# Kernel optimization log

Hardware: AMD Instinct MI355X
Metric: run time of the kernel (lower is better)

Reference implementation:

```python
import jax, jax.numpy as jnp
import numpy as np

B, S, H, NH, HD = 2, 2048, 4096, 32, 128
THETA = 10000.0


def rotate_half(x):
    x1, x2 = jnp.split(x, 2, axis=-1)
    return jnp.concatenate((-x2, x1), axis=-1)


def setup_inputs() -> dict:
    key = jax.random.key(0)
    ks = jax.random.split(key, 6)
    hidden_states = jax.random.normal(ks[0], (B, S, H), dtype=jnp.float32)
    # additive causal mask, [1,1,S,S]
    causal = jnp.triu(jnp.full((S, S), -1e9, dtype=jnp.float32), k=1)
    attention_mask = causal[None, None, :, :]
    scale = 0.02
    Wq = jax.random.normal(ks[1], (H, H), dtype=jnp.float32) * scale
    Wk = jax.random.normal(ks[2], (H, H), dtype=jnp.float32) * scale
    Wv = jax.random.normal(ks[3], (H, H), dtype=jnp.float32) * scale
    Wo = jax.random.normal(ks[4], (H, H), dtype=jnp.float32) * scale
    return {"hidden_states": hidden_states, "attention_mask": attention_mask,
            "Wq": Wq, "Wk": Wk, "Wv": Wv, "Wo": Wo}


def _rope_tables(seq_len, dtype):
    inv_freq = 1.0 / (THETA ** (jnp.arange(0, HD, 2, dtype=jnp.float32) / HD))
    t = jnp.arange(seq_len, dtype=jnp.float32)
    freqs = jnp.einsum('i,j->ij', t, inv_freq)          # [S, HD/2]
    emb = jnp.concatenate((freqs, freqs), axis=-1)       # [S, HD]
    return jnp.cos(emb).astype(dtype), jnp.sin(emb).astype(dtype)


def reference(hidden_states, attention_mask, Wq, Wk, Wv, Wo):
    b, s, _ = hidden_states.shape
    # nn.Linear: y = x @ W.T
    q = jnp.einsum('bsh,oh->bso', hidden_states, Wq).reshape(b, s, NH, HD).transpose(0, 2, 1, 3)
    k = jnp.einsum('bsh,oh->bso', hidden_states, Wk).reshape(b, s, NH, HD).transpose(0, 2, 1, 3)
    v = jnp.einsum('bsh,oh->bso', hidden_states, Wv).reshape(b, s, NH, HD).transpose(0, 2, 1, 3)
    cos, sin = _rope_tables(s, q.dtype)                  # [S, HD] broadcast over b,h
    q = q * cos + rotate_half(q) * sin
    k = k * cos + rotate_half(k) * sin
    scores = jnp.einsum('bhqd,bhkd->bhqk', q, k) / jnp.sqrt(jnp.asarray(HD, q.dtype))
    scores = scores + attention_mask
    attn = jax.nn.softmax(scores.astype(jnp.float32), axis=-1).astype(q.dtype)
    out = jnp.einsum('bhqk,bhkd->bhqd', attn, v)
    out = out.transpose(0, 2, 1, 3).reshape(b, s, H)
    return jnp.einsum('bsh,oh->bso', out, Wo)
```

## Files before the change

kernel.cpp:

```cpp
#include <hip/hip_runtime.h>
#include <stdint.h>

typedef __attribute__((ext_vector_type(4))) float f32x4;
typedef __attribute__((ext_vector_type(8))) short bf16x8;
typedef __attribute__((ext_vector_type(4))) unsigned int u32x4;

__device__ __forceinline__ short f2bf(float x) {
  unsigned int u = __builtin_bit_cast(unsigned int, x);
  unsigned int r = (u + 0x7fffu + ((u >> 16) & 1u)) >> 16;
  return (short)r;
}
__device__ __forceinline__ float bf2f(short s) {
  unsigned int u = ((unsigned int)(unsigned short)s) << 16;
  return __builtin_bit_cast(float, u);
}
__device__ __forceinline__ unsigned pkbf(float lo, float hi) {
  unsigned r;
  asm("v_cvt_pk_bf16_f32 %0, %1, %2" : "=v"(r) : "v"(lo), "v"(hi));
  return r;
}

__device__ __forceinline__ void gload_lds16(const void* g, void* l) {
  __builtin_amdgcn_global_load_lds(
      (const __attribute__((address_space(1))) void*)g,
      (__attribute__((address_space(3))) void*)l, 16, 0, 0);
}

__global__ __launch_bounds__(256) void cvt4(const float* __restrict__ a,
                                            const float* __restrict__ b,
                                            const float* __restrict__ c,
                                            const float* __restrict__ d,
                                            short* __restrict__ oa,
                                            short* __restrict__ ob,
                                            short* __restrict__ oc,
                                            short* __restrict__ od, int n) {
  const float* in = (blockIdx.y == 0) ? a : (blockIdx.y == 1) ? b : (blockIdx.y == 2) ? c : d;
  short* out = (blockIdx.y == 0) ? oa : (blockIdx.y == 1) ? ob : (blockIdx.y == 2) ? oc : od;
  int idx = blockIdx.x * blockDim.x + threadIdx.x;
  int stride = gridDim.x * blockDim.x;
  for (int i = idx * 4; i < n; i += stride * 4) {
    float4 v = *(const float4*)(in + i);
    short4 o;
    o.x = f2bf(v.x); o.y = f2bf(v.y); o.z = f2bf(v.z); o.w = f2bf(v.w);
    *(short4*)(out + i) = o;
  }
}

__global__ __launch_bounds__(256) void cvt_bf16(const float* __restrict__ in,
                                                short* __restrict__ out, int n) {
  int idx = blockIdx.x * blockDim.x + threadIdx.x;
  int stride = gridDim.x * blockDim.x;
  for (int i = idx * 4; i < n; i += stride * 4) {
    float4 v = *(const float4*)(in + i);
    short4 o;
    o.x = f2bf(v.x); o.y = f2bf(v.y); o.z = f2bf(v.z); o.w = f2bf(v.w);
    *(short4*)(out + i) = o;
  }
}

__global__ __launch_bounds__(256) void rope_table_k(float2* __restrict__ tab) {
  int idx = blockIdx.x * 256 + threadIdx.x;
  int s = idx >> 6, j = idx & 63;
  float invf = powf(10000.0f, -((float)j) / 64.0f);
  float a = (float)s * invf;
  tab[idx] = make_float2(cosf(a), sinf(a));
}

__global__ __launch_bounds__(256) void rope_apply_k(short* __restrict__ Qb,
                                                    short* __restrict__ Kb,
                                                    const float2* __restrict__ tab) {
  bool isK = (blockIdx.y != 0);
  short* base = isK ? Kb : Qb;
  float post = isK ? 1.0f : (0.08838834764831845f * 1.4426950408889634f);
  int token = blockIdx.x;
  int s = token & 2047;
  short* rowp = base + (size_t)token * 4096;
  const float2* trow = tab + s * 64;
  for (int u = threadIdx.x; u < 512; u += 256) {
    int h = u >> 4;
    int d0 = (u & 15) * 4;
    short* p1 = rowp + h * 128 + d0;
    short* p2 = p1 + 64;
    short4 a = *(short4*)p1, b = *(short4*)p2;
    short4 ra, rb;
#pragma unroll
    for (int j = 0; j < 4; ++j) {
      short aj = (&a.x)[j], bj = (&b.x)[j];
      float qa = bf2f(aj), qb = bf2f(bj);
      float2 cs = trow[d0 + j];
      (&ra.x)[j] = f2bf((qa * cs.x - qb * cs.y) * post);
      (&rb.x)[j] = f2bf((qb * cs.x + qa * cs.y) * post);
    }
    *(short4*)p1 = ra;
    *(short4*)p2 = rb;
  }
}

template <int MODE>
__global__ __launch_bounds__(512) void gemm8p(const short* __restrict__ A,
                                              const short* __restrict__ Bw,
                                              void* __restrict__ out) {
  __shared__ __attribute__((aligned(16))) short smem[2 * 32768];
  int wg = blockIdx.x;
  int xcd = wg & 7, ii = wg >> 3;
  int by = xcd * 2 + (ii >> 4);
  int bx = ii & 15;
  int tid = threadIdx.x;
  int w = tid >> 6, lane = tid & 63;
  int l16 = lane & 15, l4 = lane >> 4;
  int wm = w >> 2, wn = w & 3;

  f32x4 acc[8][4] = {};

  const short* Ab = A + (size_t)(by * 256) * 4096;
  const short* Bb = Bw + (size_t)(bx * 256) * 4096;

  auto STAGE_MAT = [&](int kt, int isB) {
    const short* src = isB ? Bb : Ab;
    int ob = (kt & 1) * 32768 + isB * 16384;
#pragma unroll
    for (int j = 0; j < 4; ++j) {
      int c = j * 512 + tid;
      int row = c >> 3;
      int sc = (c & 7) ^ (row & 7);
      gload_lds16(src + (size_t)row * 4096 + kt * 64 + sc * 8, &smem[ob + c * 8]);
    }
  };

  bf16x8 bfr[4];
  auto PHASE = [&](int ob, int kk, int mh, bool loadB) {
    const short* lA = &smem[ob];
    const short* lB = &smem[ob + 16384];
    if (loadB) {
#pragma unroll
      for (int nf = 0; nf < 4; ++nf) {
        int row = wn * 64 + nf * 16 + l16;
        int phys = (kk * 4 + l4) ^ (row & 7);
        bfr[nf] = *(const bf16x8*)&lB[row * 64 + phys * 8];
      }
    }
    bf16x8 af[4];
#pragma unroll
    for (int mf = 0; mf < 4; ++mf) {
      int row = wm * 128 + mh * 64 + mf * 16 + l16;
      int phys = (kk * 4 + l4) ^ (row & 7);
      af[mf] = *(const bf16x8*)&lA[row * 64 + phys * 8];
    }
    __builtin_amdgcn_s_setprio(1);
#pragma unroll
    for (int mf = 0; mf < 4; ++mf)
#pragma unroll
      for (int nf = 0; nf < 4; ++nf)
        acc[mh * 4 + mf][nf] =
            __builtin_amdgcn_mfma_f32_16x16x32_bf16(af[mf], bfr[nf], acc[mh * 4 + mf][nf], 0, 0, 0);
    __builtin_amdgcn_s_setprio(0);
    __builtin_amdgcn_s_barrier();
    asm volatile("" ::: "memory");
  };

  STAGE_MAT(0, 0);
  STAGE_MAT(0, 1);
  asm volatile("s_waitcnt vmcnt(0)" ::: "memory");
  __builtin_amdgcn_s_barrier();
  asm volatile("" ::: "memory");

  const int b0 = 0, b1 = 32768;
  for (int i = 0; i < 32; ++i) {
    int kt1 = 2 * i + 1;

    STAGE_MAT(kt1, 0);
    asm volatile("s_waitcnt vmcnt(4)" ::: "memory");
    __builtin_amdgcn_s_barrier();
    asm volatile("" ::: "memory");
    PHASE(b0, 0, 0, true);
    STAGE_MAT(kt1, 1);
    PHASE(b0, 0, 1, false);
    PHASE(b0, 1, 0, true);
    PHASE(b0, 1, 1, false);
    if (i + 1 < 32) {
      STAGE_MAT(2 * i + 2, 0);
      asm volatile("s_waitcnt vmcnt(4)" ::: "memory");
    } else {
      asm volatile("s_waitcnt vmcnt(0)" ::: "memory");
    }
    __builtin_amdgcn_s_barrier();
    asm volatile("" ::: "memory");
    PHASE(b1, 0, 0, true);
    if (i + 1 < 32) STAGE_MAT(2 * i + 2, 1);
    PHASE(b1, 0, 1, false);
    PHASE(b1, 1, 0, true);
    PHASE(b1, 1, 1, false);
  }

  int orow0 = by * 256 + wm * 128;
  int ocol0 = bx * 256 + wn * 64;
#pragma unroll
  for (int mf = 0; mf < 8; ++mf)
#pragma unroll
    for (int nf = 0; nf < 4; ++nf)
#pragma unroll
      for (int k = 0; k < 4; ++k) {
        int r = orow0 + mf * 16 + l4 * 4 + k;
        int c = ocol0 + nf * 16 + l16;
        float v = acc[mf][nf][k];
        if constexpr (MODE == 0) {
          ((short*)out)[(size_t)r * 4096 + c] = f2bf(v);
        } else if constexpr (MODE == 1) {
          ((float*)out)[(size_t)r * 4096 + c] = v;
        } else {
          int bb = r >> 11, ss = r & 2047;
          int h = c >> 7, d = c & 127;
          ((short*)out)[(((size_t)((bb * 32 + h) * 128 + d)) << 11) + ss] = f2bf(v);
        }
      }
}

__global__ __launch_bounds__(256) void attn_k(const short* __restrict__ Qb,
                                              const short* __restrict__ Kb,
                                              const short* __restrict__ Vt,
                                              short* __restrict__ AO) {
  __shared__ __attribute__((aligned(16))) short smem[2 * 16384];
  int p = blockIdx.x;
  int bh = p & 63;
  int qt = 15 - (p >> 6);
  int b = bh >> 5, h = bh & 31;
  int tid = threadIdx.x, w = tid >> 6, lane = tid & 63;
  int l16 = lane & 15, l4 = lane >> 4;

  const int nt = 2 * qt + 2;
  const int qbase = qt * 128 + w * 32;

  bf16x8 qf[2][4];
  {
    const short* Qg = Qb + (size_t)(b * 2048 + qbase + l16) * 4096 + h * 128 + l4 * 8;
#pragma unroll
    for (int mg = 0; mg < 2; ++mg)
#pragma unroll
      for (int kk = 0; kk < 4; ++kk)
        qf[mg][kk] = *(const bf16x8*)(Qg + (size_t)mg * 16 * 4096 + kk * 32);
  }

  f32x4 oacc[2][8] = {};
  float mrun[2] = {-1e30f, -1e30f}, lsum[2] = {0.f, 0.f};

  const short* Kbase = Kb + (size_t)(b * 2048) * 4096 + h * 128;
  const short* Vbase = Vt + (size_t)bh * 128 * 2048;

  const int srowK = l4, skbK = l16;
  const int srowV = lane >> 3, skbV = lane & 7;

  auto STAGE = [&](int t, int sel) {
    short* lK = &smem[sel * 16384];
    short* lV = lK + 8192;
#pragma unroll
    for (int ii = 0; ii < 4; ++ii) {
      int s = w * 4 + ii;
      int rowK = s * 4 + srowK;
      int srcK = skbK ^ (rowK & 15);
      gload_lds16(Kbase + (size_t)(t * 64 + rowK) * 4096 + srcK * 8, &lK[s * 512]);
      int rowV = s * 8 + srowV;
      int srcV = skbV ^ (rowV & 7);
      gload_lds16(Vbase + (size_t)rowV * 2048 + t * 64 + srcV * 8, &lV[s * 512]);
    }
  };

  STAGE(0, 0);
  __syncthreads();

  const int src0 = l16 | ((2 * (l4 & 1)) << 4);
  const int src1 = src0 | 16;
  const bool hiA = (l4 >> 1) != 0;

  for (int t = 0; t < nt; ++t) {
    int sel = t & 1;
    if (t + 1 < nt) STAGE(t + 1, sel ^ 1);
    const short* lK = &smem[sel * 16384];
    const short* lV = lK + 8192;

    bool skip = (t * 64 > qbase + 31);
    if (!skip) {
      f32x4 sacc[2][4] = {};
#pragma unroll
      for (int kk = 0; kk < 4; ++kk) {
#pragma unroll
        for (int n4 = 0; n4 < 4; ++n4) {
          int row = n4 * 16 + l16;
          int phys = (kk * 4 + l4) ^ (row & 15);
          bf16x8 kf = *(const bf16x8*)&lK[row * 128 + phys * 8];
          sacc[0][n4] = __builtin_amdgcn_mfma_f32_16x16x32_bf16(kf, qf[0][kk], sacc[0][n4], 0, 0, 0);
          sacc[1][n4] = __builtin_amdgcn_mfma_f32_16x16x32_bf16(kf, qf[1][kk], sacc[1][n4], 0, 0, 0);
        }
      }

      if (t * 64 + 63 > qbase) {
#pragma unroll
        for (int mg = 0; mg < 2; ++mg) {
          int q = qbase + mg * 16 + l16;
#pragma unroll
          for (int n4 = 0; n4 < 4; ++n4)
#pragma unroll
            for (int i = 0; i < 4; ++i) {
              int kv = t * 64 + n4 * 16 + l4 * 4 + i;
              if (kv > q) sacc[mg][n4][i] = -1e30f;
            }
        }
      }

#pragma unroll
      for (int mg = 0; mg < 2; ++mg) {
        float v0 = fmaxf(fmaxf(sacc[mg][0][0], sacc[mg][0][1]), fmaxf(sacc[mg][0][2], sacc[mg][0][3]));
        float v1 = fmaxf(fmaxf(sacc[mg][1][0], sacc[mg][1][1]), fmaxf(sacc[mg][1][2], sacc[mg][1][3]));
        float v2 = fmaxf(fmaxf(sacc[mg][2][0], sacc[mg][2][1]), fmaxf(sacc[mg][2][2], sacc[mg][2][3]));
        float v3 = fmaxf(fmaxf(sacc[mg][3][0], sacc[mg][3][1]), fmaxf(sacc[mg][3][2], sacc[mg][3][3]));
        float vm = fmaxf(fmaxf(v0, v1), fmaxf(v2, v3));
        vm = fmaxf(vm, __shfl_xor(vm, 16));
        vm = fmaxf(vm, __shfl_xor(vm, 32));
        float mn = mrun[mg];
        if (!__all(vm - mn <= 8.0f)) {
          float mnew = fmaxf(mn, vm);
          float fsc = __builtin_amdgcn_exp2f(mn - mnew);
          mrun[mg] = mnew;
          lsum[mg] *= fsc;
#pragma unroll
          for (int dg = 0; dg < 8; ++dg) oacc[mg][dg] *= fsc;
          mn = mnew;
        }
        float psum = 0.f;
#pragma unroll
        for (int n4 = 0; n4 < 4; ++n4)
#pragma unroll
          for (int i = 0; i < 4; ++i) {
            float e = __builtin_amdgcn_exp2f(sacc[mg][n4][i] - mn);
            sacc[mg][n4][i] = e;
            psum += e;
          }
        psum += __shfl_xor(psum, 16);
        psum += __shfl_xor(psum, 32);
        lsum[mg] += psum;
      }

      bf16x8 pb[2][2];
#pragma unroll
      for (int mg = 0; mg < 2; ++mg)
#pragma unroll
        for (int c = 0; c < 2; ++c) {
          unsigned pk0h0 = pkbf(sacc[mg][2 * c][0], sacc[mg][2 * c][1]);
          unsigned pk0h1 = pkbf(sacc[mg][2 * c][2], sacc[mg][2 * c][3]);
          unsigned pk1h0 = pkbf(sacc[mg][2 * c + 1][0], sacc[mg][2 * c + 1][1]);
          unsigned pk1h1 = pkbf(sacc[mg][2 * c + 1][2], sacc[mg][2 * c + 1][3]);
          unsigned s00 = __shfl((int)pk0h0, src0), s10 = __shfl((int)pk1h0, src0);
          unsigned s01 = __shfl((int)pk0h1, src0), s11 = __shfl((int)pk1h1, src0);
          unsigned t00 = __shfl((int)pk0h0, src1), t10 = __shfl((int)pk1h0, src1);
          unsigned t01 = __shfl((int)pk0h1, src1), t11 = __shfl((int)pk1h1, src1);
          u32x4 uw;
          uw[0] = hiA ? s10 : s00;
          uw[1] = hiA ? s11 : s01;
          uw[2] = hiA ? t10 : t00;
          uw[3] = hiA ? t11 : t01;
          pb[mg][c] = __builtin_bit_cast(bf16x8, uw);
        }

#pragma unroll
      for (int c = 0; c < 2; ++c)
#pragma unroll
        for (int dg = 0; dg < 8; ++dg) {
          int d = dg * 16 + l16;
          int phys = (c * 4 + l4) ^ (d & 7);
          bf16x8 vf = *(const bf16x8*)&lV[d * 64 + phys * 8];
          oacc[0][dg] = __builtin_amdgcn_mfma_f32_16x16x32_bf16(vf, pb[0][c], oacc[0][dg], 0, 0, 0);
          oacc[1][dg] = __builtin_amdgcn_mfma_f32_16x16x32_bf16(vf, pb[1][c], oacc[1][dg], 0, 0, 0);
        }
    }
    __syncthreads();
  }

  short* reg = &smem[w * 4096];
  float rls0 = 1.0f / lsum[0], rls1 = 1.0f / lsum[1];
#pragma unroll
  for (int mg = 0; mg < 2; ++mg) {
    float rls = mg ? rls1 : rls0;
    int qloc = mg * 16 + l16;
#pragma unroll
    for (int dg = 0; dg < 8; ++dg) {
      unsigned u0 = pkbf(oacc[mg][dg][0] * rls, oacc[mg][dg][1] * rls);
      unsigned u1 = pkbf(oacc[mg][dg][2] * rls, oacc[mg][dg][3] * rls);
      int c16 = dg * 2 + (l4 >> 1);
      int phys = c16 ^ (qloc & 7);
      int sidx = qloc * 128 + phys * 8 + (l4 & 1) * 4;
      *(uint2*)&reg[sidx] = make_uint2(u0, u1);
    }
  }
#pragma unroll
  for (int pass = 0; pass < 8; ++pass) {
    int qloc = pass * 4 + l4;
    int phys = l16 ^ (qloc & 7);
    bf16x8 v = *(const bf16x8*)&reg[qloc * 128 + phys * 8];
    int qg = qt * 128 + w * 32 + qloc;
    *(bf16x8*)(AO + (size_t)(b * 2048 + qg) * 4096 + h * 128 + l16 * 8) = v;
  }
}

extern "C" void kernel_launch(void* const* d_in, const int* in_sizes, int n_in,
                              void* d_out, int out_size, void* d_ws, size_t ws_size,
                              hipStream_t stream) {
  const float* X = (const float*)d_in[0];
  const float* Wq = (const float*)d_in[2];
  const float* Wk = (const float*)d_in[3];
  const float* Wv = (const float*)d_in[4];
  const float* Wo = (const float*)d_in[5];

  char* ws = (char*)d_ws;
  const size_t SEG = 32ull << 20;
  short* Xb  = (short*)(ws + 0 * SEG);
  short* Wqb = (short*)(ws + 1 * SEG);
  short* Wkb = (short*)(ws + 2 * SEG);
  short* Wvb = (short*)(ws + 3 * SEG);
  short* Qb  = (short*)(ws + 4 * SEG);
  short* Kb  = (short*)(ws + 5 * SEG);
  float2* tab = (float2*)(ws + 6 * SEG);

  const int NE = 4096 * 4096;
  cvt4<<<dim3(2048, 4), 256, 0, stream>>>(X, Wq, Wk, Wv, Xb, Wqb, Wkb, Wvb, NE);
  rope_table_k<<<512, 256, 0, stream>>>(tab);

  gemm8p<0><<<256, 512, 0, stream>>>(Xb, Wqb, Qb);
  gemm8p<0><<<256, 512, 0, stream>>>(Xb, Wkb, Kb);
  short* Vtb = Wqb;
  gemm8p<2><<<256, 512, 0, stream>>>(Xb, Wvb, Vtb);

  rope_apply_k<<<dim3(4096, 2), 256, 0, stream>>>(Qb, Kb, tab);

  short* AO = Xb;
  attn_k<<<1024, 256, 0, stream>>>(Qb, Kb, Vtb, AO);

  short* Wob = Wkb;
  cvt_bf16<<<2048, 256, 0, stream>>>(Wo, Wob, NE);
  gemm8p<1><<<256, 512, 0, stream>>>(AO, Wob, (float*)d_out);
}
```

Baseline: 711.6 us.

## Split K/V staging in attention and fold Wo conversion into initial cvt launch

The attention kernel now stages K and V separately. K is double-buffered two tiles ahead, while V uses a single buffer that is loaded after the PV step. Barriers and vmcnt waits are placed so that the QK/softmax work overlaps with the V load, and LDS use drops from 32K to 24K shorts, which may allow more resident blocks. Separately, the Wo fp32->bf16 conversion is merged into the initial multi-tensor convert launch when the workspace is large enough, removing one kernel launch. The risk is that the single V buffer adds extra barriers per iteration and can expose V load latency.

```diff
diff --git a/kernel.cpp b/kernel.cpp
--- a/kernel.cpp
+++ b/kernel.cpp
@@ -26,16 +26,19 @@
       (__attribute__((address_space(3))) void*)l, 16, 0, 0);
 }
 
-__global__ __launch_bounds__(256) void cvt4(const float* __restrict__ a,
+__global__ __launch_bounds__(256) void cvt5(const float* __restrict__ a,
                                             const float* __restrict__ b,
                                             const float* __restrict__ c,
                                             const float* __restrict__ d,
+                                            const float* __restrict__ e,
                                             short* __restrict__ oa,
                                             short* __restrict__ ob,
                                             short* __restrict__ oc,
-                                            short* __restrict__ od, int n) {
-  const float* in = (blockIdx.y == 0) ? a : (blockIdx.y == 1) ? b : (blockIdx.y == 2) ? c : d;
-  short* out = (blockIdx.y == 0) ? oa : (blockIdx.y == 1) ? ob : (blockIdx.y == 2) ? oc : od;
+                                            short* __restrict__ od,
+                                            short* __restrict__ oe, int n) {
+  int y = blockIdx.y;
+  const float* in = (y == 0) ? a : (y == 1) ? b : (y == 2) ? c : (y == 3) ? d : e;
+  short* out = (y == 0) ? oa : (y == 1) ? ob : (y == 2) ? oc : (y == 3) ? od : oe;
   int idx = blockIdx.x * blockDim.x + threadIdx.x;
   int stride = gridDim.x * blockDim.x;
   for (int i = idx * 4; i < n; i += stride * 4) {
@@ -167,7 +170,6 @@
   const int b0 = 0, b1 = 32768;
   for (int i = 0; i < 32; ++i) {
     int kt1 = 2 * i + 1;
-
     STAGE_MAT(kt1, 0);
     asm volatile("s_waitcnt vmcnt(4)" ::: "memory");
     __builtin_amdgcn_s_barrier();
@@ -219,7 +221,7 @@
                                               const short* __restrict__ Kb,
                                               const short* __restrict__ Vt,
                                               short* __restrict__ AO) {
-  __shared__ __attribute__((aligned(16))) short smem[2 * 16384];
+  __shared__ __attribute__((aligned(16))) short smem[24576];
   int p = blockIdx.x;
   int bh = p & 63;
   int qt = 15 - (p >> 6);
@@ -249,37 +251,45 @@
   const int srowK = l4, skbK = l16;
   const int srowV = lane >> 3, skbV = lane & 7;
 
-  auto STAGE = [&](int t, int sel) {
-    short* lK = &smem[sel * 16384];
-    short* lV = lK + 8192;
+  auto STAGE_K = [&](int t, int sel) {
+    short* lK = &smem[sel * 8192];
 #pragma unroll
     for (int ii = 0; ii < 4; ++ii) {
       int s = w * 4 + ii;
       int rowK = s * 4 + srowK;
       int srcK = skbK ^ (rowK & 15);
       gload_lds16(Kbase + (size_t)(t * 64 + rowK) * 4096 + srcK * 8, &lK[s * 512]);
+    }
+  };
+  auto STAGE_V = [&](int t) {
+    short* lV = &smem[16384];
+#pragma unroll
+    for (int ii = 0; ii < 4; ++ii) {
+      int s = w * 4 + ii;
       int rowV = s * 8 + srowV;
       int srcV = skbV ^ (rowV & 7);
       gload_lds16(Vbase + (size_t)rowV * 2048 + t * 64 + srcV * 8, &lV[s * 512]);
     }
   };
 
-  STAGE(0, 0);
-  __syncthreads();
+  STAGE_V(0);
+  STAGE_K(0, 0);
+  STAGE_K(1, 1);
+  asm volatile("s_waitcnt vmcnt(4)" ::: "memory");
+  __builtin_amdgcn_s_barrier();
+  asm volatile("" ::: "memory");
 
   const int src0 = l16 | ((2 * (l4 & 1)) << 4);
   const int src1 = src0 | 16;
   const bool hiA = (l4 >> 1) != 0;
 
   for (int t = 0; t < nt; ++t) {
-    int sel = t & 1;
-    if (t + 1 < nt) STAGE(t + 1, sel ^ 1);
-    const short* lK = &smem[sel * 16384];
-    const short* lV = lK + 8192;
-
+    const short* lK = &smem[(t & 1) * 8192];
+    const short* lV = &smem[16384];
     bool skip = (t * 64 > qbase + 31);
+
+    f32x4 sacc[2][4] = {};
     if (!skip) {
-      f32x4 sacc[2][4] = {};
 #pragma unroll
       for (int kk = 0; kk < 4; ++kk) {
 #pragma unroll
@@ -338,7 +348,16 @@
         psum += __shfl_xor(psum, 32);
         lsum[mg] += psum;
       }
-
+    }
+
+    if (t == nt - 1)
+      asm volatile("s_waitcnt vmcnt(0)" ::: "memory");
+    else
+      asm volatile("s_waitcnt vmcnt(4)" ::: "memory");
+    __builtin_amdgcn_s_barrier();
+    asm volatile("" ::: "memory");
+
+    if (!skip) {
       bf16x8 pb[2][2];
 #pragma unroll
       for (int mg = 0; mg < 2; ++mg)
@@ -371,7 +390,17 @@
           oacc[1][dg] = __builtin_amdgcn_mfma_f32_16x16x32_bf16(vf, pb[1][c], oacc[1][dg], 0, 0, 0);
         }
     }
-    __syncthreads();
+
+    __builtin_amdgcn_s_barrier();
+    asm volatile("" ::: "memory");
+    if (t + 1 < nt) STAGE_V(t + 1);
+    if (t + 2 < nt) STAGE_K(t + 2, t & 1);
+    if (t + 2 < nt)
+      asm volatile("s_waitcnt vmcnt(8)" ::: "memory");
+    else if (t + 1 < nt)
+      asm volatile("s_waitcnt vmcnt(4)" ::: "memory");
+    __builtin_amdgcn_s_barrier();
+    asm volatile("" ::: "memory");
   }
 
   short* reg = &smem[w * 4096];
@@ -419,8 +448,15 @@
   short* Kb  = (short*)(ws + 5 * SEG);
   float2* tab = (float2*)(ws + 6 * SEG);
 
+  bool bigws = ws_size >= 6 * SEG + (4ull << 20) + SEG;
+  short* WobBig = (short*)(ws + 6 * SEG + (4ull << 20));
+
   const int NE = 4096 * 4096;
-  cvt4<<<dim3(2048, 4), 256, 0, stream>>>(X, Wq, Wk, Wv, Xb, Wqb, Wkb, Wvb, NE);
+  if (bigws) {
+    cvt5<<<dim3(2048, 5), 256, 0, stream>>>(X, Wq, Wk, Wv, Wo, Xb, Wqb, Wkb, Wvb, WobBig, NE);
+  } else {
+    cvt5<<<dim3(2048, 4), 256, 0, stream>>>(X, Wq, Wk, Wv, nullptr, Xb, Wqb, Wkb, Wvb, nullptr, NE);
+  }
   rope_table_k<<<512, 256, 0, stream>>>(tab);
 
   gemm8p<0><<<256, 512, 0, stream>>>(Xb, Wqb, Qb);
@@ -433,7 +469,12 @@
   short* AO = Xb;
   attn_k<<<1024, 256, 0, stream>>>(Qb, Kb, Vtb, AO);
 
-  short* Wob = Wkb;
-  cvt_bf16<<<2048, 256, 0, stream>>>(Wo, Wob, NE);
+  short* Wob;
+  if (bigws) {
+    Wob = WobBig;
+  } else {
+    Wob = Wkb;
+    cvt_bf16<<<2048, 256, 0, stream>>>(Wo, Wob, NE);
+  }
   gemm8p<1><<<256, 512, 0, stream>>>(AO, Wob, (float*)d_out);
 }
```

Result: slower. 735.0 us (+3.3%).
